# Kernel tuning notes

Hardware: AMD Instinct MI355X
Metric: run time of the kernel (lower is better)

Reference implementation:

```python
import jax, jax.numpy as jnp
import numpy as np

N_HEADS = 32
N_KV_HEADS = 8
HEAD_DIM = 64
D_MODEL = 2048
EPS = 1e-6
THETA = 10000.0


def _rms_norm(x, w):
    # normalize over last dim (head_dim)
    norm = jax.lax.rsqrt(jnp.mean(jnp.square(x), axis=-1, keepdims=True) + EPS)
    return x * norm * w


def _rope(x):
    # x: (B, H, T, D)
    T, D = x.shape[2], x.shape[3]
    inv_freq = 1.0 / (THETA ** (jnp.arange(0, D, 2, dtype=jnp.float32) / D))
    t = jnp.arange(T, dtype=jnp.float32)
    freqs = jnp.outer(t, inv_freq)                      # (T, D/2)
    freqs = jnp.concatenate([freqs, freqs], axis=-1)    # (T, D)
    cos = jnp.cos(freqs)[None, None]                    # (1,1,T,D)
    sin = jnp.sin(freqs)[None, None]
    x1, x2 = x[..., : D // 2], x[..., D // 2 :]
    x_rot = jnp.concatenate([-x2, x1], axis=-1)
    return x * cos + x_rot * sin


def setup_inputs() -> dict:
    key = jax.random.key(0)
    ks = jax.random.split(key, 5)
    B, T = 2, 2048
    s = 0.02
    return {
        "x": jax.random.normal(ks[0], (B, T, D_MODEL), jnp.float32),
        "wq": jax.random.normal(ks[1], (D_MODEL, D_MODEL), jnp.float32) * s,
        "wk": jax.random.normal(ks[2], (N_KV_HEADS * HEAD_DIM, D_MODEL), jnp.float32) * s,
        "wv": jax.random.normal(ks[3], (N_KV_HEADS * HEAD_DIM, D_MODEL), jnp.float32) * s,
        "wo": jax.random.normal(ks[4], (D_MODEL, D_MODEL), jnp.float32) * s,
        "q_norm_w": jnp.ones((HEAD_DIM,), jnp.float32),
        "k_norm_w": jnp.ones((HEAD_DIM,), jnp.float32),
    }


def reference(x, wq, wk, wv, wo, q_norm_w, k_norm_w):
    B, T, C = x.shape
    G = N_HEADS // N_KV_HEADS

    q = (x @ wq.T).reshape(B, T, N_HEADS, HEAD_DIM).transpose(0, 2, 1, 3)      # (B,H,T,D)
    k = (x @ wk.T).reshape(B, T, N_KV_HEADS, HEAD_DIM).transpose(0, 2, 1, 3)   # (B,KH,T,D)
    v = (x @ wv.T).reshape(B, T, N_KV_HEADS, HEAD_DIM).transpose(0, 2, 1, 3)

    q = _rms_norm(q, q_norm_w)
    k = _rms_norm(k, k_norm_w)

    q = _rope(q)
    k = _rope(k)

    # GQA head-expand: each kv head repeated G times consecutively
    k = jnp.repeat(k, G, axis=1)   # (B,H,T,D)
    v = jnp.repeat(v, G, axis=1)

    scale = 1.0 / np.sqrt(HEAD_DIM)
    scores = jnp.einsum("bhqd,bhkd->bhqk", q, k) * scale
    causal = jnp.tril(jnp.ones((T, T), dtype=bool))
    scores = jnp.where(causal[None, None], scores, jnp.finfo(scores.dtype).min)
    attn = jax.nn.softmax(scores, axis=-1)
    out = jnp.einsum("bhqk,bhkd->bhqd", attn, v)   # (B,H,T,D)

    out = out.transpose(0, 2, 1, 3).reshape(B, T, C)
    return out @ wo.T
```

## Files before the change

kernel.cpp:

```cpp
#include <hip/hip_runtime.h>

typedef __bf16 bf16;
typedef __bf16 bf16x8 __attribute__((ext_vector_type(8)));
typedef float f32x4 __attribute__((ext_vector_type(4)));

#define DEV __device__ __forceinline__

DEV void gload16(const void* g, void* l) {
  __builtin_amdgcn_global_load_lds(
      (__attribute__((address_space(1))) void*)g,
      (__attribute__((address_space(3))) void*)l,
      16, 0, 0);
}

DEV unsigned pack_bf16(float a, float b) {
  union { bf16 h[2]; unsigned u; } u;
  u.h[0] = (bf16)a; u.h[1] = (bf16)b;
  return u.u;
}

__global__ __launch_bounds__(256) void cvt_f32_to_bf16(
    const float* __restrict__ in, bf16* __restrict__ out, long n) {
  long i = ((long)blockIdx.x * 256 + threadIdx.x) * 8;
  if (i + 8 > n) return;
  const float4* p = (const float4*)(in + i);
  float4 a = p[0], b = p[1];
  bf16x8 o;
  o[0] = (bf16)a.x; o[1] = (bf16)a.y; o[2] = (bf16)a.z; o[3] = (bf16)a.w;
  o[4] = (bf16)b.x; o[5] = (bf16)b.y; o[6] = (bf16)b.z; o[7] = (bf16)b.w;
  *(bf16x8*)(out + i) = o;
}

template <typename OutT>
__global__ __launch_bounds__(256) void gemm_bt(
    const bf16* __restrict__ A, const bf16* __restrict__ B, OutT* __restrict__ C,
    int M, int N, int K) {
  __shared__ bf16 As[128 * 64];
  __shared__ bf16 Bs[128 * 64];
  const int tid = threadIdx.x;
  const int lane = tid & 63;
  const int wv = tid >> 6;
  const int wm = wv >> 1, wn = wv & 1;
  const int l15 = lane & 15, l4 = lane >> 4;
  const long m0 = (long)blockIdx.y * 128;
  const long n0 = (long)blockIdx.x * 128;

  f32x4 acc[4][4];
#pragma unroll
  for (int i = 0; i < 4; ++i)
#pragma unroll
    for (int j = 0; j < 4; ++j) acc[i][j] = (f32x4){0.f, 0.f, 0.f, 0.f};

  for (int k0 = 0; k0 < K; k0 += 64) {
#pragma unroll
    for (int it = 0; it < 4; ++it) {
      const int flat = it * 256 + tid;
      const int row = flat >> 3;
      const int col = (flat & 7) * 8;
      gload16(A + (m0 + row) * (long)K + k0 + col, &As[flat * 8]);
      gload16(B + (n0 + row) * (long)K + k0 + col, &Bs[flat * 8]);
    }
    __syncthreads();
#pragma unroll
    for (int kk = 0; kk < 2; ++kk) {
      bf16x8 af[4], bfr[4];
#pragma unroll
      for (int i = 0; i < 4; ++i)
        af[i] = *(const bf16x8*)&As[(wm * 64 + i * 16 + l15) * 64 + kk * 32 + l4 * 8];
#pragma unroll
      for (int j = 0; j < 4; ++j)
        bfr[j] = *(const bf16x8*)&Bs[(wn * 64 + j * 16 + l15) * 64 + kk * 32 + l4 * 8];
#pragma unroll
      for (int i = 0; i < 4; ++i)
#pragma unroll
        for (int j = 0; j < 4; ++j)
          acc[i][j] = __builtin_amdgcn_mfma_f32_16x16x32_bf16(af[i], bfr[j], acc[i][j], 0, 0, 0);
    }
    __syncthreads();
  }

#pragma unroll
  for (int i = 0; i < 4; ++i)
#pragma unroll
    for (int j = 0; j < 4; ++j) {
      const long row = m0 + wm * 64 + i * 16 + l4 * 4;
      const long col = n0 + wn * 64 + j * 16 + l15;
#pragma unroll
      for (int r = 0; r < 4; ++r)
        C[(row + r) * (long)N + col] = (OutT)acc[i][j][r];
    }
}

__global__ __launch_bounds__(256) void qk_norm_rope(
    const bf16* __restrict__ qkv, const float* __restrict__ qw,
    const float* __restrict__ kw, bf16* __restrict__ Qh, bf16* __restrict__ Kh) {
  const int wg = blockIdx.x * 4 + (threadIdx.x >> 6);
  const int lane = threadIdx.x & 63;
  const int row = wg / 40;
  const int head = wg - row * 40;
  const int b = row >> 11, t = row & 2047;
  const bool is_q = head < 32;
  const int col0 = is_q ? head * 64 : 2048 + (head - 32) * 64;

  float v = (float)qkv[(long)row * 3072 + col0 + lane];
  float ss = v * v;
  ss += __shfl_xor(ss, 1);
  ss += __shfl_xor(ss, 2);
  ss += __shfl_xor(ss, 4);
  ss += __shfl_xor(ss, 8);
  ss += __shfl_xor(ss, 16);
  ss += __shfl_xor(ss, 32);
  const float norm = rsqrtf(ss * (1.0f / 64.0f) + 1e-6f);
  const float* wn = is_q ? qw : kw;
  float xn = v * norm * wn[lane];

  const int fi = lane & 31;
  const float inv_freq = expf(-(float)fi * (9.210340371976184f / 32.0f));
  const float fr = (float)t * inv_freq;
  float sn, cs;
  sincosf(fr, &sn, &cs);
  const float xo = __shfl_xor(xn, 32);
  const float xr = (lane < 32) ? -xo : xo;
  const float res = xn * cs + xr * sn;

  if (is_q)
    Qh[(((long)b * 32 + head) * 2048 + t) * 64 + lane] = (bf16)res;
  else
    Kh[(((long)b * 8 + (head - 32)) * 2048 + t) * 64 + lane] = (bf16)res;
}

__global__ __launch_bounds__(256) void v_transpose(
    const bf16* __restrict__ qkv, bf16* __restrict__ Vt) {
  const int bh = blockIdx.x;
  const int t0 = blockIdx.y * 64;
  const int b = bh >> 3, kh = bh & 7;
  __shared__ bf16 tile[64][72];
  const int tid = threadIdx.x;
#pragma unroll
  for (int it = 0; it < 2; ++it) {
    const int tt = it * 32 + (tid >> 3);
    const int d0 = (tid & 7) * 8;
    bf16x8 val = *(const bf16x8*)&qkv[((long)b * 2048 + t0 + tt) * 3072 + 2560 + kh * 64 + d0];
#pragma unroll
    for (int j = 0; j < 8; ++j) tile[tt][d0 + j] = val[j];
  }
  __syncthreads();
#pragma unroll
  for (int it = 0; it < 2; ++it) {
    const int d = it * 32 + (tid >> 3);
    const int tb = (tid & 7) * 8;
    bf16x8 o;
#pragma unroll
    for (int j = 0; j < 8; ++j) o[j] = tile[tb + j][d];
    *(bf16x8*)&Vt[((long)bh * 64 + d) * 2048 + t0 + tb] = o;
  }
}

__global__ __launch_bounds__(256, 4) void attn_fwd(
    const bf16* __restrict__ Q, const bf16* __restrict__ K,
    const bf16* __restrict__ Vt, bf16* __restrict__ O) {
  const int b = blockIdx.x >> 5, h = blockIdx.x & 31;
  const int qb = 31 - (int)blockIdx.y;
  const int q0 = qb * 64;
  const int kvh = h >> 2;
  const bf16* Qp = Q + (((long)b * 32 + h) * 2048 + q0) * 64;
  const bf16* Kp = K + ((long)b * 8 + kvh) * (2048L * 64);
  const bf16* Vp = Vt + ((long)b * 8 + kvh) * (64L * 2048);

  __shared__ bf16 Ks[64 * 64];
  __shared__ bf16 Vs[64 * 64];

  const int tid = threadIdx.x, lane = tid & 63, w = tid >> 6;
  const int l15 = lane & 15, l4 = lane >> 4;
  const int qwr = q0 + w * 16;
  const int q_g = qwr + l15;

  bf16x8 qf[2];
#pragma unroll
  for (int kk = 0; kk < 2; ++kk)
    qf[kk] = *(const bf16x8*)(Qp + (w * 16 + l15) * 64 + kk * 32 + l4 * 8);

  f32x4 accO[4];
#pragma unroll
  for (int dn = 0; dn < 4; ++dn) accO[dn] = (f32x4){0.f, 0.f, 0.f, 0.f};
  float M = -1e30f, L = 0.f;

  const float scale = 0.125f;
  const int swz = (l15 & 7) << 3;

  for (int kt = 0; kt <= qb; ++kt) {
    const int k0 = kt * 64;
#pragma unroll
    for (int it = 0; it < 2; ++it) {
      const int c = it * 256 + tid;
      const int row = c >> 3, cc = c & 7;
      const int scol = ((cc ^ (row & 7)) << 3);
      gload16(Kp + (long)(k0 + row) * 64 + scol, &Ks[c * 8]);
      gload16(Vp + (long)row * 2048 + k0 + scol, &Vs[c * 8]);
    }
    __syncthreads();

    f32x4 sT[4];
#pragma unroll
    for (int n = 0; n < 4; ++n) sT[n] = (f32x4){0.f, 0.f, 0.f, 0.f};
#pragma unroll
    for (int kk = 0; kk < 2; ++kk) {
      bf16x8 kf[4];
#pragma unroll
      for (int n = 0; n < 4; ++n)
        kf[n] = *(const bf16x8*)&Ks[(n * 16 + l15) * 64 + (((kk * 4 + l4) << 3) ^ swz)];
#pragma unroll
      for (int n = 0; n < 4; ++n)
        sT[n] = __builtin_amdgcn_mfma_f32_16x16x32_bf16(kf[n], qf[kk], sT[n], 0, 0, 0);
    }

    const bool edge = (kt == qb);
#pragma unroll
    for (int n = 0; n < 4; ++n) {
      const int kbase = k0 + n * 16 + l4 * 4;
#pragma unroll
      for (int r = 0; r < 4; ++r) {
        float v = sT[n][r] * scale;
        if (edge && (kbase + r > q_g)) v = -1e30f;
        sT[n][r] = v;
      }
    }

    float pm = -1e30f;
#pragma unroll
    for (int n = 0; n < 4; ++n)
#pragma unroll
      for (int r = 0; r < 4; ++r) pm = fmaxf(pm, sT[n][r]);
    pm = fmaxf(pm, __shfl_xor(pm, 16));
    pm = fmaxf(pm, __shfl_xor(pm, 32));
    const float newM = fmaxf(M, pm);
    const float sc = __expf(M - newM);
    M = newM;
    float rs = 0.f;
#pragma unroll
    for (int n = 0; n < 4; ++n)
#pragma unroll
      for (int r = 0; r < 4; ++r) {
        const float pv = __expf(sT[n][r] - newM);
        sT[n][r] = pv;
        rs += pv;
      }
    rs += __shfl_xor(rs, 16);
    rs += __shfl_xor(rs, 32);
    L = L * sc + rs;
#pragma unroll
    for (int dn = 0; dn < 4; ++dn) accO[dn] *= sc;

    unsigned lo[4], hi[4];
#pragma unroll
    for (int n = 0; n < 4; ++n) {
      lo[n] = pack_bf16(sT[n][0], sT[n][1]);
      hi[n] = pack_bf16(sT[n][2], sT[n][3]);
    }

    const int srcA = l15 | ((l4 & 1) << 5);
    const int srcB = srcA + 16;
    const bool selHi = (l4 >> 1);
#pragma unroll
    for (int kk = 0; kk < 2; ++kk) {
      unsigned d0a = __shfl(lo[2 * kk], srcA), d0b = __shfl(lo[2 * kk + 1], srcA);
      unsigned d1a = __shfl(hi[2 * kk], srcA), d1b = __shfl(hi[2 * kk + 1], srcA);
      unsigned d2a = __shfl(lo[2 * kk], srcB), d2b = __shfl(lo[2 * kk + 1], srcB);
      unsigned d3a = __shfl(hi[2 * kk], srcB), d3b = __shfl(hi[2 * kk + 1], srcB);
      union { unsigned d[4]; bf16x8 v; } pu;
      pu.d[0] = selHi ? d0b : d0a;
      pu.d[1] = selHi ? d1b : d1a;
      pu.d[2] = selHi ? d2b : d2a;
      pu.d[3] = selHi ? d3b : d3a;
      bf16x8 vf[4];
#pragma unroll
      for (int dn = 0; dn < 4; ++dn)
        vf[dn] = *(const bf16x8*)&Vs[(dn * 16 + l15) * 64 + (((kk * 4 + l4) << 3) ^ swz)];
#pragma unroll
      for (int dn = 0; dn < 4; ++dn)
        accO[dn] = __builtin_amdgcn_mfma_f32_16x16x32_bf16(vf[dn], pu.v, accO[dn], 0, 0, 0);
    }
    __syncthreads();
  }

  const float inv = 1.0f / L;
  const long rowbase = ((long)b * 2048 + q_g) * 2048 + h * 64;
#pragma unroll
  for (int dn = 0; dn < 4; ++dn)
#pragma unroll
    for (int rp = 0; rp < 2; ++rp) {
      const unsigned pk = pack_bf16(accO[dn][2 * rp] * inv, accO[dn][2 * rp + 1] * inv);
      *(unsigned*)&O[rowbase + dn * 16 + l4 * 4 + 2 * rp] = pk;
    }
}

extern "C" void kernel_launch(void* const* d_in, const int* in_sizes, int n_in,
                              void* d_out, int out_size, void* d_ws, size_t ws_size,
                              hipStream_t stream) {
  const float* x   = (const float*)d_in[0];
  const float* wq  = (const float*)d_in[1];
  const float* wk  = (const float*)d_in[2];
  const float* wv  = (const float*)d_in[3];
  const float* wo  = (const float*)d_in[4];
  const float* qnw = (const float*)d_in[5];
  const float* knw = (const float*)d_in[6];
  float* out = (float*)d_out;

  char* ws = (char*)d_ws;
  size_t off = 0;
  auto carve = [&](size_t bytes) -> void* {
    void* p = ws + off;
    off += (bytes + 255) & ~(size_t)255;
    return p;
  };
  bf16* xb    = (bf16*)carve(8388608ull * 2);
  bf16* wqkvb = (bf16*)carve(6291456ull * 2);
  bf16* wob   = (bf16*)carve(4194304ull * 2);
  bf16* qkvb  = (bf16*)carve(12582912ull * 2);
  bf16* Qh    = (bf16*)carve(8388608ull * 2);
  bf16* Kh    = (bf16*)carve(2097152ull * 2);
  bf16* Vt    = (bf16*)carve(2097152ull * 2);

  cvt_f32_to_bf16<<<4096, 256, 0, stream>>>(x, xb, 8388608L);
  cvt_f32_to_bf16<<<2048, 256, 0, stream>>>(wq, wqkvb, 4194304L);
  cvt_f32_to_bf16<<<512, 256, 0, stream>>>(wk, wqkvb + 4194304, 1048576L);
  cvt_f32_to_bf16<<<512, 256, 0, stream>>>(wv, wqkvb + 5242880, 1048576L);
  cvt_f32_to_bf16<<<2048, 256, 0, stream>>>(wo, wob, 4194304L);

  gemm_bt<bf16><<<dim3(24, 32), 256, 0, stream>>>(xb, wqkvb, qkvb, 4096, 3072, 2048);
  qk_norm_rope<<<40960, 256, 0, stream>>>(qkvb, qnw, knw, Qh, Kh);
  v_transpose<<<dim3(16, 32), 256, 0, stream>>>(qkvb, Vt);

  bf16* attnb = xb;
  attn_fwd<<<dim3(64, 32), 256, 0, stream>>>(Qh, Kh, Vt, attnb);

  gemm_bt<float><<<dim3(16, 32), 256, 0, stream>>>(attnb, wob, out, 4096, 2048, 2048);
}
```

Baseline: 376.2 us.

## Replace GEMM with 256x256 double-buffered, swizzled, 8-wave phased pipeline

Replaces the simple 128x128 single-buffered GEMM with a 256x256-tile, 512-thread kernel. It double-buffers A and B in LDS, uses an XOR swizzle to avoid bank conflicts, and splits each K-step into four phases that interleave the next tile's global-to-LDS loads with MFMA work, using explicit barriers, waitcnts and priority changes. This targets exposed load latency and LDS bank conflicts in both projection GEMMs. In exchange it launches far fewer blocks (192 and 128 workgroups on a 256-CU part), which risks leaving CUs idle. It also uses 128KB of LDS per block and relies on hand-tuned wait counts.

```diff
diff --git a/kernel.cpp b/kernel.cpp
--- a/kernel.cpp
+++ b/kernel.cpp
@@ -32,58 +32,120 @@
 }
 
 template <typename OutT>
-__global__ __launch_bounds__(256) void gemm_bt(
+__global__ __launch_bounds__(512, 2) void gemm8p(
     const bf16* __restrict__ A, const bf16* __restrict__ B, OutT* __restrict__ C,
     int M, int N, int K) {
-  __shared__ bf16 As[128 * 64];
-  __shared__ bf16 Bs[128 * 64];
+  __shared__ bf16 As[2][256 * 64];
+  __shared__ bf16 Bs[2][256 * 64];
   const int tid = threadIdx.x;
   const int lane = tid & 63;
   const int wv = tid >> 6;
-  const int wm = wv >> 1, wn = wv & 1;
+  const int wm = wv >> 2, wn = wv & 3;
   const int l15 = lane & 15, l4 = lane >> 4;
-  const long m0 = (long)blockIdx.y * 128;
-  const long n0 = (long)blockIdx.x * 128;
-
-  f32x4 acc[4][4];
-#pragma unroll
-  for (int i = 0; i < 4; ++i)
+  const int swz7 = l15 & 7;
+  const long m0 = (long)blockIdx.y * 256;
+  const long n0 = (long)blockIdx.x * 256;
+  const int NT = K >> 6;
+
+  f32x4 acc[8][4];
+#pragma unroll
+  for (int i = 0; i < 8; ++i)
 #pragma unroll
     for (int j = 0; j < 4; ++j) acc[i][j] = (f32x4){0.f, 0.f, 0.f, 0.f};
 
-  for (int k0 = 0; k0 < K; k0 += 64) {
-#pragma unroll
-    for (int it = 0; it < 4; ++it) {
-      const int flat = it * 256 + tid;
-      const int row = flat >> 3;
-      const int col = (flat & 7) * 8;
-      gload16(A + (m0 + row) * (long)K + k0 + col, &As[flat * 8]);
-      gload16(B + (n0 + row) * (long)K + k0 + col, &Bs[flat * 8]);
-    }
-    __syncthreads();
-#pragma unroll
-    for (int kk = 0; kk < 2; ++kk) {
-      bf16x8 af[4], bfr[4];
-#pragma unroll
-      for (int i = 0; i < 4; ++i)
-        af[i] = *(const bf16x8*)&As[(wm * 64 + i * 16 + l15) * 64 + kk * 32 + l4 * 8];
-#pragma unroll
-      for (int j = 0; j < 4; ++j)
-        bfr[j] = *(const bf16x8*)&Bs[(wn * 64 + j * 16 + l15) * 64 + kk * 32 + l4 * 8];
-#pragma unroll
-      for (int i = 0; i < 4; ++i)
-#pragma unroll
-        for (int j = 0; j < 4; ++j)
-          acc[i][j] = __builtin_amdgcn_mfma_f32_16x16x32_bf16(af[i], bfr[j], acc[i][j], 0, 0, 0);
-    }
-    __syncthreads();
-  }
-
-#pragma unroll
-  for (int i = 0; i < 4; ++i)
+  auto stageA = [&](int t, int q) {
+#pragma unroll
+    for (int it = 0; it < 2; ++it) {
+      const int c = it * 512 + tid;
+      const int row = ((c >> 9) << 7) + q * 64 + ((c >> 3) & 63);
+      const int cc = c & 7;
+      gload16(A + (m0 + row) * (long)K + t * 64 + ((cc ^ (row & 7)) << 3),
+              &As[t & 1][row * 64 + cc * 8]);
+    }
+  };
+  auto stageB = [&](int t, int q) {
+#pragma unroll
+    for (int it = 0; it < 2; ++it) {
+      const int c = it * 512 + tid;
+      const int row = ((c >> 8) << 6) + q * 32 + ((c >> 3) & 31);
+      const int cc = c & 7;
+      gload16(B + (n0 + row) * (long)K + t * 64 + ((cc ^ (row & 7)) << 3),
+              &Bs[t & 1][row * 64 + cc * 8]);
+    }
+  };
+
+#define PHASE(CUR, QM, QN, STAGE, VM) do {                                      \
+    __builtin_amdgcn_sched_barrier(0);                                          \
+    bf16x8 af_[2][4], bf_[2][2];                                                \
+    _Pragma("unroll")                                                           \
+    for (int kk = 0; kk < 2; ++kk) {                                            \
+      _Pragma("unroll")                                                         \
+      for (int i = 0; i < 4; ++i)                                               \
+        af_[kk][i] = *(const bf16x8*)&As[CUR][                                  \
+            (wm * 128 + (QM) * 64 + i * 16 + l15) * 64 +                        \
+            (((kk * 4 + l4) ^ swz7) << 3)];                                     \
+      _Pragma("unroll")                                                         \
+      for (int j = 0; j < 2; ++j)                                               \
+        bf_[kk][j] = *(const bf16x8*)&Bs[CUR][                                  \
+            (wn * 64 + (QN) * 32 + j * 16 + l15) * 64 +                         \
+            (((kk * 4 + l4) ^ swz7) << 3)];                                     \
+    }                                                                           \
+    STAGE;                                                                      \
+    VM;                                                                         \
+    __builtin_amdgcn_sched_barrier(0);                                          \
+    __builtin_amdgcn_s_barrier();                                               \
+    asm volatile("s_waitcnt lgkmcnt(0)" ::: "memory");                          \
+    __builtin_amdgcn_sched_barrier(0);                                          \
+    __builtin_amdgcn_s_setprio(1);                                              \
+    _Pragma("unroll")                                                           \
+    for (int kk = 0; kk < 2; ++kk)                                              \
+      _Pragma("unroll")                                                         \
+      for (int i = 0; i < 4; ++i)                                               \
+        _Pragma("unroll")                                                       \
+        for (int j = 0; j < 2; ++j)                                             \
+          acc[(QM) * 4 + i][(QN) * 2 + j] =                                     \
+              __builtin_amdgcn_mfma_f32_16x16x32_bf16(                          \
+                  af_[kk][i], bf_[kk][j], acc[(QM) * 4 + i][(QN) * 2 + j],      \
+                  0, 0, 0);                                                     \
+    __builtin_amdgcn_s_setprio(0);                                              \
+    __builtin_amdgcn_s_barrier();                                               \
+  } while (0)
+
+  stageA(0, 0); stageA(0, 1); stageB(0, 0); stageB(0, 1);
+  stageA(1, 0); stageB(1, 0);
+  asm volatile("s_waitcnt vmcnt(4)" ::: "memory");
+  __builtin_amdgcn_sched_barrier(0);
+  __builtin_amdgcn_s_barrier();
+
+  for (int T = 0; T < NT - 2; ++T) {
+    const int cur = T & 1;
+    PHASE(cur, 0, 0, stageA(T + 1, 1), );
+    PHASE(cur, 0, 1, stageB(T + 1, 1), );
+    PHASE(cur, 1, 0, stageA(T + 2, 0), );
+    PHASE(cur, 1, 1, stageB(T + 2, 0),
+          asm volatile("s_waitcnt vmcnt(4)" ::: "memory"));
+  }
+  {
+    const int cur = (NT - 2) & 1;
+    PHASE(cur, 0, 0, stageA(NT - 1, 1), );
+    PHASE(cur, 0, 1, stageB(NT - 1, 1), );
+    PHASE(cur, 1, 0, , );
+    PHASE(cur, 1, 1, , asm volatile("s_waitcnt vmcnt(0)" ::: "memory"));
+  }
+  {
+    const int cur = (NT - 1) & 1;
+    PHASE(cur, 0, 0, , );
+    PHASE(cur, 0, 1, , );
+    PHASE(cur, 1, 0, , );
+    PHASE(cur, 1, 1, , );
+  }
+#undef PHASE
+
+#pragma unroll
+  for (int i = 0; i < 8; ++i)
 #pragma unroll
     for (int j = 0; j < 4; ++j) {
-      const long row = m0 + wm * 64 + i * 16 + l4 * 4;
+      const long row = m0 + wm * 128 + i * 16 + l4 * 4;
       const long col = n0 + wn * 64 + j * 16 + l15;
 #pragma unroll
       for (int r = 0; r < 4; ++r)
@@ -327,12 +389,12 @@
   cvt_f32_to_bf16<<<512, 256, 0, stream>>>(wv, wqkvb + 5242880, 1048576L);
   cvt_f32_to_bf16<<<2048, 256, 0, stream>>>(wo, wob, 4194304L);
 
-  gemm_bt<bf16><<<dim3(24, 32), 256, 0, stream>>>(xb, wqkvb, qkvb, 4096, 3072, 2048);
+  gemm8p<bf16><<<dim3(12, 16), 512, 0, stream>>>(xb, wqkvb, qkvb, 4096, 3072, 2048);
   qk_norm_rope<<<40960, 256, 0, stream>>>(qkvb, qnw, knw, Qh, Kh);
   v_transpose<<<dim3(16, 32), 256, 0, stream>>>(qkvb, Vt);
 
   bf16* attnb = xb;
   attn_fwd<<<dim3(64, 32), 256, 0, stream>>>(Qh, Kh, Vt, attnb);
 
-  gemm_bt<float><<<dim3(16, 32), 256, 0, stream>>>(attnb, wob, out, 4096, 2048, 2048);
-}
+  gemm8p<float><<<dim3(8, 16), 512, 0, stream>>>(attnb, wob, out, 4096, 2048, 2048);
+}
```

New measurement: 389.0 us. 1.03x slower.
